# Kernel optimization log

Measured on AMD Instinct MI355X. Metric: run time of the kernel, lower is better.

Reference implementation:

```python
import jax, jax.numpy as jnp
import numpy as np


def _box_avg(x, k, p):
    # F.avg_pool2d(x, kernel_size=k, stride=1, padding=p) with count_include_pad=True:
    # zero-padded window sum divided by k*k everywhere.
    s = jax.lax.reduce_window(x, 0.0, jax.lax.add,
                              (1, 1, k, k), (1, 1, 1, 1),
                              ((0, 0), (0, 0), (p, p), (p, p)))
    return s / float(k * k)


def setup_inputs() -> dict:
    key = jax.random.key(0)
    k1, k2 = jax.random.split(key)
    B, C, H, W = 32, 1, 384, 384
    EPS = 1e-4  # keep pred strictly inside (0,1) for BCE logs
    pred = jax.random.uniform(k1, (B, C, H, W), jnp.float32, EPS, 1.0 - EPS)
    mask = jax.random.uniform(k2, (B, C, H, W), jnp.float32)
    return {"pred": pred, "mask": mask}


def reference(pred, mask):
    # multi-scale boundary-aware weight
    w1 = jnp.abs(_box_avg(mask, 3, 1) - mask)
    w2 = jnp.abs(_box_avg(mask, 15, 7) - mask)
    w3 = jnp.abs(_box_avg(mask, 31, 15) - mask)
    weit = 1.0 + 0.5 * (w1 + w2 + w3) * mask  # [B,C,H,W]

    # F.binary_cross_entropy(..., reduction='mean') -> scalar
    bce = -(mask * jnp.log(pred) + (1.0 - mask) * jnp.log(1.0 - pred)).mean()
    wsum = weit.sum(axis=(2, 3))  # [B,C]
    wbce = (weit * bce).sum(axis=(2, 3)) / wsum  # == bce broadcast, kept faithful

    inter = (pred * mask * weit).sum(axis=(2, 3))
    union = ((pred + mask) * weit).sum(axis=(2, 3))
    wiou = 1.0 - inter / (union - inter)

    # F.l1_loss(pred, mask, reduce=None) resolves to mean reduction -> scalar
    mae = jnp.abs(pred - mask).mean()
    wmae = (weit * mae).sum(axis=(2, 3)) / (weit - 1.0).sum(axis=(2, 3))

    return (0.7 * wbce + 0.7 * wiou + 0.7 * wmae).mean()
```

## Files before the change

### kernel.cpp

```cpp
#include <hip/hip_runtime.h>
#include <hip/hip_fp16.h>
#include <math.h>

#define W 384
#define H 384
#define NB 32
#define NPIX (W*H)

#define BAND 16
#define NBANDS (H/BAND)
#define NBLK1 (NB*NBANDS)
#define LSTR 416

#define RC 6
#define CPI 96
#define NBLK2 (NB*CPI)

__global__ __launch_bounds__(384) void band_v_kernel(
    const float* __restrict__ mask,
    __half* __restrict__ V3, __half* __restrict__ V15, __half* __restrict__ V31)
{
    __shared__ float lds[BAND][LSTR];

    const int tid  = threadIdx.x;
    const int wave = tid >> 6;
    const int lane = tid & 63;
    const int bid  = blockIdx.x;
    const int b    = (bid & 7) + 8 * ((bid >> 3) / NBANDS);
    const int band = (bid >> 3) % NBANDS;
    const int y0   = band * BAND;

    const float* mimg = mask + (size_t)b * NPIX;

    if (tid < 256) { lds[tid >> 4][tid & 15] = 0.0f; }

    {
        const int x0 = lane * 6;
        #pragma unroll
        for (int i = 0; i < 3; ++i) {
            const int r = wave + i * 6;
            if (r < BAND) {
                const float2* src = (const float2*)(mimg + (size_t)(y0 + r) * W + x0);
                const float2 q0 = src[0], q1 = src[1], q2 = src[2];
                const float s0 = q0.x;
                const float s1 = s0 + q0.y;
                const float s2 = s1 + q1.x;
                const float s3 = s2 + q1.y;
                const float s4 = s3 + q2.x;
                const float s5 = s4 + q2.y;
                float ss = s5;
                #pragma unroll
                for (int d = 1; d < 64; d <<= 1) {
                    float t = __shfl_up(ss, d);
                    if (lane >= d) ss += t;
                }
                const float base = ss - s5;
                float2* dst = (float2*)&lds[r][16 + x0];
                dst[0] = make_float2(base + s0, base + s1);
                dst[1] = make_float2(base + s2, base + s3);
                dst[2] = make_float2(base + s4, base + s5);
            }
        }
    }
    __syncthreads();

    {
        const int c = 16 + tid;
        float v[BAND];
        #pragma unroll
        for (int r = 0; r < BAND; ++r) v[r] = lds[r][c];
        float acc = 0.0f;
        #pragma unroll
        for (int r = 0; r < BAND; ++r) { acc += v[r]; v[r] = acc; }
        #pragma unroll
        for (int r = 0; r < BAND; ++r) lds[r][c] = v[r];
    }
    __syncthreads();

    if (tid < 256) {
        const int r = tid >> 4, j = tid & 15;
        lds[r][400 + j] = lds[r][399];
    }
    __syncthreads();

    {
        const int cp = tid % 192;
        const int hf = tid / 192;
        const int c0 = 16 + 2 * cp;
        const size_t obase = (size_t)b * NPIX + (size_t)y0 * W + 2 * cp;
        #pragma unroll
        for (int rr = 0; rr < 8; ++rr) {
            const int r = hf * 8 + rr;
            const float* R = lds[r];
            const __half2 h3  = __floats2half2_rn(R[c0+1]  - R[c0-2],  R[c0+2]  - R[c0-1]);
            const __half2 h15 = __floats2half2_rn(R[c0+7]  - R[c0-8],  R[c0+8]  - R[c0-7]);
            const __half2 h31 = __floats2half2_rn(R[c0+15] - R[c0-16], R[c0+16] - R[c0-15]);
            const size_t o = obase + (size_t)r * W;
            *(__half2*)(V3  + o) = h3;
            *(__half2*)(V15 + o) = h15;
            *(__half2*)(V31 + o) = h31;
        }
    }
}

__global__ __launch_bounds__(128) void loss_kernel(
    const float* __restrict__ pred, const float* __restrict__ mask,
    const __half* __restrict__ V3, const __half* __restrict__ V15,
    const __half* __restrict__ V31, float* __restrict__ partials)
{
    const int tid  = threadIdx.x;
    const int wave = tid >> 6;
    const int lane = tid & 63;
    const int bid  = blockIdx.x;
    const int b    = (bid & 7) + 8 * ((bid >> 3) / CPI);
    const int qq   = (bid >> 3) % CPI;
    const int widx = qq * 2 + wave;
    const int cg   = widx % 3;
    const int rcid = widx / 3;
    const int x    = cg * 128 + 2 * lane;
    const int yA   = rcid * RC;

    const __half* v3i  = V3  + (size_t)b * NPIX + x;
    const __half* v15i = V15 + (size_t)b * NPIX + x;
    const __half* v31i = V31 + (size_t)b * NPIX + x;
    const float*  mi   = mask + (size_t)b * NPIX + x;
    const float*  pi_  = pred + (size_t)b * NPIX + x;

    float pw = 0.f, pin = 0.f, pun = 0.f, pb = 0.f, pm = 0.f;
    const float i9 = 1.0f/9.0f, i225 = 1.0f/225.0f, i961 = 1.0f/961.0f;

    #pragma unroll
    for (int i = 0; i < RC; ++i) {
        const int y = yA + i;

        float b3a, b3b, b15a, b15b, b31a, b31b;
        #define RAD_BOX3(r, vp, h0, h1)                                          \
        {                                                                        \
            const int y1  = min(y + (r), H - 1);                                 \
            const int ylo = y - (r) - 1;                                         \
            const int y0c = ylo < 0 ? 0 : ylo;                                   \
            const int ytp = y0c | (BAND - 1);                                    \
            const float fLo = ylo >= 0 ? 1.0f : 0.0f;                            \
            const float fC  = (ylo >= 0 && (y0c >> 4) != (y1 >> 4)) ? 1.0f : 0.0f; \
            const float2 f1 = __half22float2(*(const __half2*)(vp + (size_t)y1  * W)); \
            const float2 f0 = __half22float2(*(const __half2*)(vp + (size_t)y0c * W)); \
            const float2 ft = __half22float2(*(const __half2*)(vp + (size_t)ytp * W)); \
            h0 = f1.x - fLo * f0.x + fC * ft.x;                                  \
            h1 = f1.y - fLo * f0.y + fC * ft.y;                                  \
        }
        RAD_BOX3(1, v3i,  b3a,  b3b)
        RAD_BOX3(7, v15i, b15a, b15b)
        #undef RAD_BOX3
        {
            const int y1  = min(y + 15, H - 1);
            const int ylo = y - 16;
            const int y0c = ylo < 0 ? 0 : ylo;
            const int s   = ylo >= 0 ? (y0c >> 4) : 0;
            const int n   = (y1 >> 4) - s;
            const int rt1 = s * BAND + (BAND - 1);
            const int rt2 = min(rt1 + BAND, H - 1);
            const float fLo = ylo >= 0 ? 1.0f : 0.0f;
            const float g1  = n >= 1 ? 1.0f : 0.0f;
            const float g2  = n >= 2 ? 1.0f : 0.0f;
            const float2 f1 = __half22float2(*(const __half2*)(v31i + (size_t)y1  * W));
            const float2 f0 = __half22float2(*(const __half2*)(v31i + (size_t)y0c * W));
            const float2 t1 = __half22float2(*(const __half2*)(v31i + (size_t)rt1 * W));
            const float2 t2 = __half22float2(*(const __half2*)(v31i + (size_t)rt2 * W));
            b31a = f1.x - fLo * f0.x + g1 * t1.x + g2 * t2.x;
            b31b = f1.y - fLo * f0.y + g1 * t1.y + g2 * t2.y;
        }

        const float2 mv = *(const float2*)(mi  + (size_t)y * W);
        const float2 pv = *(const float2*)(pi_ + (size_t)y * W);
        {
            const float m = mv.x, p = pv.x;
            const float w = fabsf(b3a*i9 - m) + fabsf(b15a*i225 - m) + fabsf(b31a*i961 - m);
            const float weit = 1.0f + 0.5f * w * m;
            pw += weit; pin += p*m*weit; pun += (p+m)*weit;
            pb -= m*__logf(p) + (1.0f - m)*__logf(1.0f - p);
            pm += fabsf(p - m);
        }
        {
            const float m = mv.y, p = pv.y;
            const float w = fabsf(b3b*i9 - m) + fabsf(b15b*i225 - m) + fabsf(b31b*i961 - m);
            const float weit = 1.0f + 0.5f * w * m;
            pw += weit; pin += p*m*weit; pun += (p+m)*weit;
            pb -= m*__logf(p) + (1.0f - m)*__logf(1.0f - p);
            pm += fabsf(p - m);
        }
    }

    #pragma unroll
    for (int off = 32; off >= 1; off >>= 1) {
        pw  += __shfl_xor(pw,  off);
        pin += __shfl_xor(pin, off);
        pun += __shfl_xor(pun, off);
        pb  += __shfl_xor(pb,  off);
        pm  += __shfl_xor(pm,  off);
    }
    __shared__ float red[2][5];
    if (lane == 0) {
        red[wave][0]=pw; red[wave][1]=pin; red[wave][2]=pun; red[wave][3]=pb; red[wave][4]=pm;
    }
    __syncthreads();
    if (tid == 0) {
        float* o = partials + (size_t)bid * 8;
        o[0]=red[0][0]+red[1][0]; o[1]=red[0][1]+red[1][1]; o[2]=red[0][2]+red[1][2];
        o[3]=red[0][3]+red[1][3]; o[4]=red[0][4]+red[1][4];
    }
}

__global__ __launch_bounds__(256) void finalize_kernel(
    const float* __restrict__ partials, float* __restrict__ out)
{
    __shared__ double sB[4], sM[4];
    __shared__ double sw_[NB], si_[NB], su_[NB];

    const int t = threadIdx.x;
    const int i = t >> 3;
    const int s = t & 7;

    double Sw=0, Si=0, Su=0, Bc=0, Ma=0;
    for (int k = s; k < CPI; k += 8) {
        const int bid = (i & 7) + (((i >> 3) * CPI + k) << 3);
        const float* pp = partials + (size_t)bid * 8;
        Sw += (double)pp[0]; Si += (double)pp[1]; Su += (double)pp[2];
        Bc += (double)pp[3]; Ma += (double)pp[4];
    }
    #pragma unroll
    for (int d = 4; d >= 1; d >>= 1) {
        Sw += __shfl_down(Sw, d);
        Si += __shfl_down(Si, d);
        Su += __shfl_down(Su, d);
    }
    if (s == 0) { sw_[i] = Sw; si_[i] = Si; su_[i] = Su; }

    #pragma unroll
    for (int d = 32; d >= 1; d >>= 1) {
        Bc += __shfl_down(Bc, d);
        Ma += __shfl_down(Ma, d);
    }
    if ((t & 63) == 0) { sB[t >> 6] = Bc; sM[t >> 6] = Ma; }
    __syncthreads();

    if (t < 64) {
        double wiou = 0.0, ratio = 0.0;
        if (t < NB) {
            const double w = sw_[t], ii = si_[t], u = su_[t];
            wiou  = 1.0 - ii / (u - ii);
            ratio = w / (w - (double)NPIX);
        }
        #pragma unroll
        for (int d = 32; d >= 1; d >>= 1) {
            wiou  += __shfl_down(wiou,  d);
            ratio += __shfl_down(ratio, d);
        }
        if (t == 0) {
            const double bt  = sB[0]+sB[1]+sB[2]+sB[3];
            const double mt  = sM[0]+sM[1]+sM[2]+sM[3];
            const double tot = (double)NB * (double)NPIX;
            const double bce = bt / tot;
            const double mae = mt / tot;
            out[0] = (float)(0.7 * (bce + wiou/(double)NB + mae * ratio/(double)NB));
        }
    }
}

extern "C" void kernel_launch(void* const* d_in, const int* in_sizes, int n_in,
                              void* d_out, int out_size, void* d_ws, size_t ws_size,
                              hipStream_t stream) {
    const float* pred = (const float*)d_in[0];
    const float* mask = (const float*)d_in[1];
    float* out        = (float*)d_out;

    const size_t vplane = (size_t)NB * NPIX;
    __half* V3  = (__half*)d_ws;
    __half* V15 = V3  + vplane;
    __half* V31 = V15 + vplane;
    float* partials = (float*)(V31 + vplane);

    band_v_kernel<<<dim3(NBLK1), dim3(384), 0, stream>>>(mask, V3, V15, V31);
    loss_kernel<<<dim3(NBLK2), dim3(128), 0, stream>>>(pred, mask, V3, V15, V31, partials);
    finalize_kernel<<<dim3(1), dim3(256), 0, stream>>>(partials, out);
}
```

Baseline: 34.60 us.

## Fuse finalize into loss kernel via last-block atomic and widen loads

Removes the separate finalize launch. Each loss block bumps an atomic counter, and the last block to finish does the final double-precision reduction. The loss kernel is also restructured: 256-thread blocks, each lane processes 4 contiguous pixels with 8-byte half loads and float4 mask/pred loads, over 3 iterations across a 768-pixel chunk. The counter is reset inside the first kernel. This adds a threadfence and atomic per block and a serialized tail reduction in one block.

```diff
diff --git a/kernel.cpp b/kernel.cpp
--- a/kernel.cpp
+++ b/kernel.cpp
@@ -12,13 +12,14 @@
 #define NBLK1 (NB*NBANDS)
 #define LSTR 416
 
-#define RC 6
-#define CPI 96
-#define NBLK2 (NB*CPI)
+#define NBLK2 1536
+#define CGPI 48
+#define ITERS 3
 
 __global__ __launch_bounds__(384) void band_v_kernel(
     const float* __restrict__ mask,
-    __half* __restrict__ V3, __half* __restrict__ V15, __half* __restrict__ V31)
+    __half* __restrict__ V3, __half* __restrict__ V15, __half* __restrict__ V31,
+    unsigned* __restrict__ counter)
 {
     __shared__ float lds[BAND][LSTR];
 
@@ -29,6 +30,8 @@
     const int b    = (bid & 7) + 8 * ((bid >> 3) / NBANDS);
     const int band = (bid >> 3) % NBANDS;
     const int y0   = band * BAND;
+
+    if (bid == 0 && tid == 0) *counter = 0u;
 
     const float* mimg = mask + (size_t)b * NPIX;
 
@@ -103,55 +106,76 @@
     }
 }
 
-__global__ __launch_bounds__(128) void loss_kernel(
+struct __align__(8) H4 { __half2 a, b; };
+
+__device__ inline void vtap(const __half* vp, int row, float o[4]) {
+    const H4 h = *(const H4*)(vp + (size_t)row * W);
+    const float2 fa = __half22float2(h.a);
+    const float2 fb = __half22float2(h.b);
+    o[0] = fa.x; o[1] = fa.y; o[2] = fb.x; o[3] = fb.y;
+}
+
+__global__ __launch_bounds__(256) void loss_kernel(
     const float* __restrict__ pred, const float* __restrict__ mask,
     const __half* __restrict__ V3, const __half* __restrict__ V15,
-    const __half* __restrict__ V31, float* __restrict__ partials)
+    const __half* __restrict__ V31, float* __restrict__ partials,
+    unsigned* __restrict__ counter, float* __restrict__ out)
 {
     const int tid  = threadIdx.x;
     const int wave = tid >> 6;
     const int lane = tid & 63;
     const int bid  = blockIdx.x;
-    const int b    = (bid & 7) + 8 * ((bid >> 3) / CPI);
-    const int qq   = (bid >> 3) % CPI;
-    const int widx = qq * 2 + wave;
-    const int cg   = widx % 3;
-    const int rcid = widx / 3;
-    const int x    = cg * 128 + 2 * lane;
-    const int yA   = rcid * RC;
-
-    const __half* v3i  = V3  + (size_t)b * NPIX + x;
-    const __half* v15i = V15 + (size_t)b * NPIX + x;
-    const __half* v31i = V31 + (size_t)b * NPIX + x;
-    const float*  mi   = mask + (size_t)b * NPIX + x;
-    const float*  pi_  = pred + (size_t)b * NPIX + x;
+    const int j    = bid >> 3;
+    const int b    = (bid & 7) + 8 * (j / CGPI);
+    const int cg   = j % CGPI;
+    const int chunk = cg * 4 + wave;
+
+    const size_t ibase = (size_t)b * NPIX;
+    const float* mimg = mask + ibase;
+    const float* pimg = pred + ibase;
 
     float pw = 0.f, pin = 0.f, pun = 0.f, pb = 0.f, pm = 0.f;
     const float i9 = 1.0f/9.0f, i225 = 1.0f/225.0f, i961 = 1.0f/961.0f;
 
     #pragma unroll
-    for (int i = 0; i < RC; ++i) {
-        const int y = yA + i;
-
-        float b3a, b3b, b15a, b15b, b31a, b31b;
-        #define RAD_BOX3(r, vp, h0, h1)                                          \
-        {                                                                        \
-            const int y1  = min(y + (r), H - 1);                                 \
-            const int ylo = y - (r) - 1;                                         \
-            const int y0c = ylo < 0 ? 0 : ylo;                                   \
-            const int ytp = y0c | (BAND - 1);                                    \
-            const float fLo = ylo >= 0 ? 1.0f : 0.0f;                            \
-            const float fC  = (ylo >= 0 && (y0c >> 4) != (y1 >> 4)) ? 1.0f : 0.0f; \
-            const float2 f1 = __half22float2(*(const __half2*)(vp + (size_t)y1  * W)); \
-            const float2 f0 = __half22float2(*(const __half2*)(vp + (size_t)y0c * W)); \
-            const float2 ft = __half22float2(*(const __half2*)(vp + (size_t)ytp * W)); \
-            h0 = f1.x - fLo * f0.x + fC * ft.x;                                  \
-            h1 = f1.y - fLo * f0.y + fC * ft.y;                                  \
-        }
-        RAD_BOX3(1, v3i,  b3a,  b3b)
-        RAD_BOX3(7, v15i, b15a, b15b)
-        #undef RAD_BOX3
+    for (int it = 0; it < ITERS; ++it) {
+        const int q  = it * 256 + (lane << 2);
+        const int yo = (q >= 384) ? 1 : 0;
+        const int y  = (chunk << 1) + yo;
+        const int x  = q - (yo ? 384 : 0);
+        const size_t po = (size_t)chunk * 768 + q;
+
+        const __half* v3x  = V3  + ibase + x;
+        const __half* v15x = V15 + ibase + x;
+        const __half* v31x = V31 + ibase + x;
+
+        float b3v[4], b15v[4], b31v[4];
         {
+            float t1[4], t0[4], tt[4];
+            const int y1  = min(y + 1, H - 1);
+            const int ylo = y - 2;
+            const int y0c = ylo < 0 ? 0 : ylo;
+            const int ytp = y0c | (BAND - 1);
+            const float fLo = ylo >= 0 ? 1.0f : 0.0f;
+            const float fC  = (ylo >= 0 && (y0c >> 4) != (y1 >> 4)) ? 1.0f : 0.0f;
+            vtap(v3x, y1, t1); vtap(v3x, y0c, t0); vtap(v3x, ytp, tt);
+            #pragma unroll
+            for (int c = 0; c < 4; ++c) b3v[c] = t1[c] - fLo * t0[c] + fC * tt[c];
+        }
+        {
+            float t1[4], t0[4], tt[4];
+            const int y1  = min(y + 7, H - 1);
+            const int ylo = y - 8;
+            const int y0c = ylo < 0 ? 0 : ylo;
+            const int ytp = y0c | (BAND - 1);
+            const float fLo = ylo >= 0 ? 1.0f : 0.0f;
+            const float fC  = (ylo >= 0 && (y0c >> 4) != (y1 >> 4)) ? 1.0f : 0.0f;
+            vtap(v15x, y1, t1); vtap(v15x, y0c, t0); vtap(v15x, ytp, tt);
+            #pragma unroll
+            for (int c = 0; c < 4; ++c) b15v[c] = t1[c] - fLo * t0[c] + fC * tt[c];
+        }
+        {
+            float t1[4], t0[4], ta[4], tb[4];
             const int y1  = min(y + 15, H - 1);
             const int ylo = y - 16;
             const int y0c = ylo < 0 ? 0 : ylo;
@@ -162,31 +186,27 @@
             const float fLo = ylo >= 0 ? 1.0f : 0.0f;
             const float g1  = n >= 1 ? 1.0f : 0.0f;
             const float g2  = n >= 2 ? 1.0f : 0.0f;
-            const float2 f1 = __half22float2(*(const __half2*)(v31i + (size_t)y1  * W));
-            const float2 f0 = __half22float2(*(const __half2*)(v31i + (size_t)y0c * W));
-            const float2 t1 = __half22float2(*(const __half2*)(v31i + (size_t)rt1 * W));
-            const float2 t2 = __half22float2(*(const __half2*)(v31i + (size_t)rt2 * W));
-            b31a = f1.x - fLo * f0.x + g1 * t1.x + g2 * t2.x;
-            b31b = f1.y - fLo * f0.y + g1 * t1.y + g2 * t2.y;
-        }
-
-        const float2 mv = *(const float2*)(mi  + (size_t)y * W);
-        const float2 pv = *(const float2*)(pi_ + (size_t)y * W);
-        {
-            const float m = mv.x, p = pv.x;
-            const float w = fabsf(b3a*i9 - m) + fabsf(b15a*i225 - m) + fabsf(b31a*i961 - m);
+            vtap(v31x, y1, t1); vtap(v31x, y0c, t0); vtap(v31x, rt1, ta); vtap(v31x, rt2, tb);
+            #pragma unroll
+            for (int c = 0; c < 4; ++c)
+                b31v[c] = t1[c] - fLo * t0[c] + g1 * ta[c] + g2 * tb[c];
+        }
+
+        const float4 mv = *(const float4*)(mimg + po);
+        const float4 pv = *(const float4*)(pimg + po);
+        const float mm[4] = { mv.x, mv.y, mv.z, mv.w };
+        const float pp[4] = { pv.x, pv.y, pv.z, pv.w };
+
+        #pragma unroll
+        for (int c = 0; c < 4; ++c) {
+            const float m = mm[c], p = pp[c];
+            const float w = fabsf(b3v[c]*i9 - m) + fabsf(b15v[c]*i225 - m) + fabsf(b31v[c]*i961 - m);
             const float weit = 1.0f + 0.5f * w * m;
-            pw += weit; pin += p*m*weit; pun += (p+m)*weit;
-            pb -= m*__logf(p) + (1.0f - m)*__logf(1.0f - p);
-            pm += fabsf(p - m);
-        }
-        {
-            const float m = mv.y, p = pv.y;
-            const float w = fabsf(b3b*i9 - m) + fabsf(b15b*i225 - m) + fabsf(b31b*i961 - m);
-            const float weit = 1.0f + 0.5f * w * m;
-            pw += weit; pin += p*m*weit; pun += (p+m)*weit;
-            pb -= m*__logf(p) + (1.0f - m)*__logf(1.0f - p);
-            pm += fabsf(p - m);
+            pw  += weit;
+            pin += p * m * weit;
+            pun += (p + m) * weit;
+            pb  -= m * __logf(p) + (1.0f - m) * __logf(1.0f - p);
+            pm  += fabsf(p - m);
         }
     }
 
@@ -198,34 +218,44 @@
         pb  += __shfl_xor(pb,  off);
         pm  += __shfl_xor(pm,  off);
     }
-    __shared__ float red[2][5];
+    __shared__ float red[4][5];
     if (lane == 0) {
         red[wave][0]=pw; red[wave][1]=pin; red[wave][2]=pun; red[wave][3]=pb; red[wave][4]=pm;
     }
     __syncthreads();
     if (tid == 0) {
-        float* o = partials + (size_t)bid * 8;
-        o[0]=red[0][0]+red[1][0]; o[1]=red[0][1]+red[1][1]; o[2]=red[0][2]+red[1][2];
-        o[3]=red[0][3]+red[1][3]; o[4]=red[0][4]+red[1][4];
-    }
-}
-
-__global__ __launch_bounds__(256) void finalize_kernel(
-    const float* __restrict__ partials, float* __restrict__ out)
-{
+        float* o = partials + (size_t)(b * CGPI + cg) * 8;
+        o[0]=red[0][0]+red[1][0]+red[2][0]+red[3][0];
+        o[1]=red[0][1]+red[1][1]+red[2][1]+red[3][1];
+        o[2]=red[0][2]+red[1][2]+red[2][2]+red[3][2];
+        o[3]=red[0][3]+red[1][3]+red[2][3]+red[3][3];
+        o[4]=red[0][4]+red[1][4]+red[2][4]+red[3][4];
+    }
+
+    __shared__ int lastFlag;
+    if (tid == 0) {
+        __threadfence();
+        const unsigned old = atomicAdd(counter, 1u);
+        lastFlag = (old == (unsigned)(NBLK2 - 1)) ? 1 : 0;
+    }
+    __syncthreads();
+    if (!lastFlag) return;
+    __threadfence();
+
     __shared__ double sB[4], sM[4];
     __shared__ double sw_[NB], si_[NB], su_[NB];
 
-    const int t = threadIdx.x;
-    const int i = t >> 3;
-    const int s = t & 7;
-
-    double Sw=0, Si=0, Su=0, Bc=0, Ma=0;
-    for (int k = s; k < CPI; k += 8) {
-        const int bid = (i & 7) + (((i >> 3) * CPI + k) << 3);
-        const float* pp = partials + (size_t)bid * 8;
-        Sw += (double)pp[0]; Si += (double)pp[1]; Su += (double)pp[2];
-        Bc += (double)pp[3]; Ma += (double)pp[4];
+    const int i = tid >> 3;
+    const int s = tid & 7;
+
+    double Sw = 0, Si = 0, Su = 0, Bc = 0, Ma = 0;
+    for (int k = s; k < CGPI; k += 8) {
+        const float* q = partials + (size_t)(i * CGPI + k) * 8;
+        Sw += (double)q[0]; Si += (double)q[1]; Su += (double)q[2];
+    }
+    for (int k = tid; k < NBLK2; k += 256) {
+        const float* q = partials + (size_t)k * 8;
+        Bc += (double)q[3]; Ma += (double)q[4];
     }
     #pragma unroll
     for (int d = 4; d >= 1; d >>= 1) {
@@ -234,19 +264,18 @@
         Su += __shfl_down(Su, d);
     }
     if (s == 0) { sw_[i] = Sw; si_[i] = Si; su_[i] = Su; }
-
     #pragma unroll
     for (int d = 32; d >= 1; d >>= 1) {
         Bc += __shfl_down(Bc, d);
         Ma += __shfl_down(Ma, d);
     }
-    if ((t & 63) == 0) { sB[t >> 6] = Bc; sM[t >> 6] = Ma; }
-    __syncthreads();
-
-    if (t < 64) {
+    if ((tid & 63) == 0) { sB[tid >> 6] = Bc; sM[tid >> 6] = Ma; }
+    __syncthreads();
+
+    if (tid < 64) {
         double wiou = 0.0, ratio = 0.0;
-        if (t < NB) {
-            const double w = sw_[t], ii = si_[t], u = su_[t];
+        if (tid < NB) {
+            const double w = sw_[tid], ii = si_[tid], u = su_[tid];
             wiou  = 1.0 - ii / (u - ii);
             ratio = w / (w - (double)NPIX);
         }
@@ -255,13 +284,13 @@
             wiou  += __shfl_down(wiou,  d);
             ratio += __shfl_down(ratio, d);
         }
-        if (t == 0) {
-            const double bt  = sB[0]+sB[1]+sB[2]+sB[3];
-            const double mt  = sM[0]+sM[1]+sM[2]+sM[3];
+        if (tid == 0) {
+            const double bt  = sB[0] + sB[1] + sB[2] + sB[3];
+            const double mt  = sM[0] + sM[1] + sM[2] + sM[3];
             const double tot = (double)NB * (double)NPIX;
             const double bce = bt / tot;
             const double mae = mt / tot;
-            out[0] = (float)(0.7 * (bce + wiou/(double)NB + mae * ratio/(double)NB));
+            out[0] = (float)(0.7 * (bce + wiou / (double)NB + mae * ratio / (double)NB));
         }
     }
 }
@@ -278,8 +307,9 @@
     __half* V15 = V3  + vplane;
     __half* V31 = V15 + vplane;
     float* partials = (float*)(V31 + vplane);
-
-    band_v_kernel<<<dim3(NBLK1), dim3(384), 0, stream>>>(mask, V3, V15, V31);
-    loss_kernel<<<dim3(NBLK2), dim3(128), 0, stream>>>(pred, mask, V3, V15, V31, partials);
-    finalize_kernel<<<dim3(1), dim3(256), 0, stream>>>(partials, out);
+    unsigned* counter = (unsigned*)(partials + (size_t)NBLK2 * 8);
+
+    band_v_kernel<<<dim3(NBLK1), dim3(384), 0, stream>>>(mask, V3, V15, V31, counter);
+    loss_kernel<<<dim3(NBLK2), dim3(256), 0, stream>>>(pred, mask, V3, V15, V31,
+                                                       partials, counter, out);
 }
```

After: 76.09 us. +119.9%, slower.
